# Kernel optimization log

Hardware: AMD Instinct MI355X
Metric: run time of the kernel (lower is better)

## Reference

```python
import jax, jax.numpy as jnp
import numpy as np

N_NODES = 100_000
N_EDGES = 1_600_000
N_GRAPHS = 256          # num_segments for batch scatter (static)
T_CAPS = 16             # num_target_cap
IN_CH = 64
OUT_CH = 64
NUM_ROUTES = 3
BN_EPS = 1e-5


def squash(s, axis=-1):
    # v = (|s|^2 / (1+|s|^2)) * s / |s|
    sq = jnp.sum(s * s, axis=axis, keepdims=True)
    return (sq / (1.0 + sq)) * s / jnp.sqrt(sq + 1e-16)


def setup_inputs() -> dict:
    key = jax.random.key(0)
    k_x, k_ei, k_ew, k_b, k_w, k_bias = jax.random.split(key, 6)
    x = jax.random.normal(k_x, (N_NODES, IN_CH), dtype=jnp.float32)
    edge_index = jax.random.randint(k_ei, (2, N_EDGES), 0, N_NODES, dtype=jnp.int32)
    edge_weight = jax.random.uniform(k_ew, (N_EDGES,), dtype=jnp.float32)
    batch = jnp.sort(jax.random.randint(k_b, (N_NODES,), 0, N_GRAPHS, dtype=jnp.int32))
    # per-capsule GCNConv weights, stacked: (T, in, out), bias (T, out)
    W = jax.random.normal(k_w, (T_CAPS, IN_CH, OUT_CH), dtype=jnp.float32) * 0.05
    bias = jax.random.normal(k_bias, (T_CAPS, OUT_CH), dtype=jnp.float32) * 0.05
    bn_gamma = jnp.ones((IN_CH,), dtype=jnp.float32)
    bn_beta = jnp.zeros((IN_CH,), dtype=jnp.float32)
    return {"x": x, "edge_index": edge_index, "edge_weight": edge_weight,
            "batch": batch, "bn_gamma": bn_gamma, "bn_beta": bn_beta,
            "W": W, "bias": bias}


def reference(x, edge_index, edge_weight, batch, bn_gamma, bn_beta, W, bias):
    N = x.shape[0]
    T = W.shape[0]
    # --- BatchNorm1d (training-mode batch statistics, biased variance) ---
    mu = jnp.mean(x, axis=0)
    var = jnp.var(x, axis=0)
    xn = (x - mu) * jax.lax.rsqrt(var + BN_EPS) * bn_gamma + bn_beta

    # --- GCNConv (shared graph): A_hat x, then per-capsule linear ---
    row, col = edge_index[0], edge_index[1]
    ar = jnp.arange(N, dtype=edge_index.dtype)
    row_f = jnp.concatenate([row, ar])              # add self-loops, weight 1
    col_f = jnp.concatenate([col, ar])
    w_f = jnp.concatenate([edge_weight, jnp.ones((N,), x.dtype)])
    deg = jax.ops.segment_sum(w_f, col_f, num_segments=N)
    dinv = jnp.where(deg > 0, jax.lax.rsqrt(deg), 0.0)
    norm = dinv[row_f] * w_f * dinv[col_f]          # (E+N,)
    h = jax.ops.segment_sum(norm[:, None] * xn[row_f], col_f, num_segments=N)  # (N, in)
    # linearity: propagate(A, x W_t) == (propagate(A, x)) W_t
    u_hat = jnp.einsum('ni,tio->nto', h, W) + bias[None]  # (N, T, D)

    # --- dynamic routing ---
    node_deg = jax.ops.segment_sum(edge_weight, row, num_segments=N)  # (N,)
    b_log = jnp.broadcast_to(node_deg[:, None, None], (N, T, 1))
    u_det = jax.lax.stop_gradient(u_hat)
    for _ in range(NUM_ROUTES - 1):
        c = jax.nn.softmax(b_log, axis=1)                         # (N, T, 1)
        s = jax.ops.segment_sum(c * u_det, batch, num_segments=N_GRAPHS)  # (G, T, D)
        v = squash(s, axis=-1)
        vg = v[batch]                                             # (N, T, D)
        b_log = b_log + jnp.sum(u_det * vg, axis=-1, keepdims=True)
    c = jax.nn.softmax(b_log, axis=1)
    s = jax.ops.segment_sum(c * u_hat, batch, num_segments=N_GRAPHS)  # (G, T, D)

    # --- add per-graph mean of (normalized) node features ---
    cnt = jax.ops.segment_sum(jnp.ones((N,), x.dtype), batch, num_segments=N_GRAPHS)
    x_mean = jax.ops.segment_sum(xn, batch, num_segments=N_GRAPHS) / jnp.maximum(cnt, 1.0)[:, None]
    s = s + x_mean[:, None, :]                                    # needs in==out
    v = squash(s, axis=-1)

    # --- final_layer=True: v.norm(p=-1, dim=-1) = (sum |v|^-1)^-1 ---
    out = 1.0 / jnp.sum(1.0 / jnp.abs(v), axis=-1)                # (G, T)
    return out
```

## Files before the change

### kernel.cpp

```cpp
#include <hip/hip_runtime.h>
#include <hip/hip_fp16.h>
#include <math.h>

#define N_NODES 100000
#define N_EDGES 1600000
#define N_GRAPHS 256
#define T_CAPS 16
#define D_CH 64
#define BN_EPS 1e-5f
#define NSPLIT 8
#define CHUNK 32
#define FIX_SCALE 33554432.0f

__device__ __forceinline__ float waveReduceSum(float v) {
    for (int m = 32; m >= 1; m >>= 1) v += __shfl_xor(v, m, 64);
    return v;
}

__global__ void setup_kernel(unsigned long long* pack, float* bn_sums, float* hsum, float* xsum,
                             const float* __restrict__ W, float* __restrict__ WT,
                             const int* __restrict__ batch, int* __restrict__ gstart) {
    int idx = blockIdx.x * blockDim.x + threadIdx.x;
    if (idx < N_NODES) pack[idx] = 0ULL;
    if (idx < 128) bn_sums[idx] = 0.0f;
    if (idx < N_GRAPHS * D_CH) { hsum[idx] = 0.0f; xsum[idx] = 0.0f; }
    if (idx < T_CAPS * 64 * 64) {
        int t = idx >> 12, rem = idx & 4095, o = rem >> 6, i = rem & 63;
        WT[idx] = W[t * 4096 + i * 64 + o];
    }
    if (idx <= N_GRAPHS) {
        int lo = 0, hi = N_NODES;
        while (lo < hi) { int mid = (lo + hi) >> 1; if (batch[mid] < idx) lo = mid + 1; else hi = mid; }
        gstart[idx] = lo;
    }
}

__global__ void bn_stats_kernel(const float* __restrict__ x, float* __restrict__ sums,
                                __half2* __restrict__ x16) {
    int pr = threadIdx.x & 31;
    int rg = threadIdx.x >> 5;
    int c0 = pr * 2;
    float s0 = 0, q0 = 0, s1 = 0, q1 = 0;
    for (int r = blockIdx.x * 8 + rg; r < N_NODES; r += gridDim.x * 8) {
        float2 v = *(const float2*)(x + (size_t)r * 64 + c0);
        s0 += v.x; q0 += v.x * v.x;
        s1 += v.y; q1 += v.y * v.y;
        x16[(size_t)r * 32 + pr] = __floats2half2_rn(v.x, v.y);
    }
    __shared__ float ls[2][8][64];
    ls[0][rg][c0] = s0; ls[0][rg][c0 + 1] = s1;
    ls[1][rg][c0] = q0; ls[1][rg][c0 + 1] = q1;
    __syncthreads();
    if (threadIdx.x < 64) {
        float a = 0.0f, b = 0.0f;
        for (int i = 0; i < 8; i++) { a += ls[0][i][threadIdx.x]; b += ls[1][i][threadIdx.x]; }
        atomicAdd(&sums[threadIdx.x], a);
        atomicAdd(&sums[64 + threadIdx.x], b);
    }
}

__global__ void hist_kernel(const int* __restrict__ col, const float* __restrict__ ew,
                            unsigned long long* __restrict__ pack, int* __restrict__ rank) {
    int e = blockIdx.x * blockDim.x + threadIdx.x;
    if (e >= N_EDGES) return;
    int c = col[e];
    unsigned fx = __float2uint_rn(ew[e] * FIX_SCALE);
    unsigned long long old = atomicAdd(&pack[c], (1ULL << 32) | (unsigned long long)fx);
    rank[e] = (int)(old >> 32);
}

__global__ void scan1_kernel(const unsigned long long* __restrict__ pack, int* __restrict__ off,
                             int* __restrict__ bsum, float* __restrict__ dinv,
                             const float* __restrict__ sums, const float* __restrict__ gamma,
                             const float* __restrict__ beta, float* __restrict__ ab) {
    __shared__ int lds[256];
    int tid = threadIdx.x;
    int base = blockIdx.x * 1024 + tid * 4;
    int c[4];
    #pragma unroll
    for (int i = 0; i < 4; i++) {
        if (base + i < N_NODES) {
            unsigned long long pv = pack[base + i];
            c[i] = (int)(pv >> 32);
            float d = 1.0f + (float)(unsigned)(pv & 0xFFFFFFFFULL) * (1.0f / FIX_SCALE);
            dinv[base + i] = 1.0f / sqrtf(d);
        } else c[i] = 0;
    }
    if (blockIdx.x == 0 && tid < 64) {
        float mu = sums[tid] * (1.0f / N_NODES);
        float var = sums[64 + tid] * (1.0f / N_NODES) - mu * mu;
        float inv = 1.0f / sqrtf(var + BN_EPS);
        float a = inv * gamma[tid];
        ab[tid] = a;
        ab[64 + tid] = beta[tid] - mu * a;
    }
    int tsum = c[0] + c[1] + c[2] + c[3];
    lds[tid] = tsum;
    __syncthreads();
    for (int d = 1; d < 256; d <<= 1) {
        int v = (tid >= d) ? lds[tid - d] : 0;
        __syncthreads();
        lds[tid] += v;
        __syncthreads();
    }
    int excl = lds[tid] - tsum;
    if (base + 0 < N_NODES) off[base + 0] = excl;
    if (base + 1 < N_NODES) off[base + 1] = excl + c[0];
    if (base + 2 < N_NODES) off[base + 2] = excl + c[0] + c[1];
    if (base + 3 < N_NODES) off[base + 3] = excl + c[0] + c[1] + c[2];
    if (tid == 255) bsum[blockIdx.x] = lds[255];
}

__global__ void scan2_kernel(int* __restrict__ bsum, int nb) {
    __shared__ int lds[128];
    int tid = threadIdx.x;
    int v = (tid < nb) ? bsum[tid] : 0;
    lds[tid] = v;
    __syncthreads();
    for (int d = 1; d < 128; d <<= 1) {
        int u = (tid >= d) ? lds[tid - d] : 0;
        __syncthreads();
        lds[tid] += u;
        __syncthreads();
    }
    if (tid < nb) bsum[tid] = lds[tid] - v;
}

__global__ void scan3_kernel(int* __restrict__ off, const int* __restrict__ bsum) {
    int idx = blockIdx.x * blockDim.x + threadIdx.x;
    if (idx < N_NODES) off[idx] = off[idx] + bsum[idx >> 10];
    if (idx == 0) off[N_NODES] = N_EDGES;
}

__global__ void scatter_kernel(const int* __restrict__ row, const int* __restrict__ col,
                               const float* __restrict__ ew, const int* __restrict__ rank,
                               const float* __restrict__ dinv, const int* __restrict__ off,
                               int2* __restrict__ rec) {
    int e = blockIdx.x * blockDim.x + threadIdx.x;
    if (e >= N_EDGES) return;
    int c = col[e], r = row[e];
    float coef = dinv[r] * ew[e] * dinv[c];
    int pos = off[c] + rank[e];
    rec[pos] = make_int2(r, __float_as_int(coef));
}

__global__ void h_gather_kernel(const int2* __restrict__ rec, const int* __restrict__ off,
                                const float* __restrict__ dinv, const __half* __restrict__ x16,
                                const float* __restrict__ ab, float* __restrict__ h) {
    int n = blockIdx.x * 4 + (threadIdx.x >> 6);
    int ch = threadIdx.x & 63;
    int e0 = off[n], e1 = off[n + 1];
    float dv = dinv[n];
    float cself = dv * dv;
    float acc0 = cself * __half2float(x16[(size_t)n * 64 + ch]);
    float acc1 = 0.0f, acc2 = 0.0f, acc3 = 0.0f;
    float csr = cself;
    int e = e0;
    for (; e + 4 <= e1; e += 4) {
        int2 r0 = rec[e], r1 = rec[e + 1], r2 = rec[e + 2], r3 = rec[e + 3];
        float c0 = __int_as_float(r0.y), c1 = __int_as_float(r1.y);
        float c2 = __int_as_float(r2.y), c3 = __int_as_float(r3.y);
        float x0 = __half2float(x16[(size_t)r0.x * 64 + ch]);
        float x1 = __half2float(x16[(size_t)r1.x * 64 + ch]);
        float x2 = __half2float(x16[(size_t)r2.x * 64 + ch]);
        float x3 = __half2float(x16[(size_t)r3.x * 64 + ch]);
        acc0 += c0 * x0; acc1 += c1 * x1; acc2 += c2 * x2; acc3 += c3 * x3;
        csr += c0 + c1 + c2 + c3;
    }
    for (; e < e1; ++e) {
        int2 rc = rec[e];
        float c = __int_as_float(rc.y);
        acc0 += c * __half2float(x16[(size_t)rc.x * 64 + ch]);
        csr += c;
    }
    float acc = (acc0 + acc1) + (acc2 + acc3);
    h[(size_t)n * 64 + ch] = ab[ch] * acc + ab[64 + ch] * csr;
}

__global__ void gsum_kernel(const __half* __restrict__ x16, const float* __restrict__ h,
                            const int* __restrict__ gstart, float* __restrict__ xsum,
                            float* __restrict__ hsum) {
    int g = blockIdx.x / NSPLIT, sp = blockIdx.x % NSPLIT;
    int s0g = gstart[g], s1g = gstart[g + 1];
    int len = s1g - s0g;
    int q = (len + NSPLIT - 1) / NSPLIT;
    int a0 = s0g + sp * q, a1 = min(s1g, a0 + q);
    int ch = threadIdx.x & 63, rg = threadIdx.x >> 6;
    float ax = 0.0f, ah = 0.0f;
    for (int n = a0 + rg; n < a1; n += 4) {
        ax += __half2float(x16[(size_t)n * 64 + ch]);
        ah += h[(size_t)n * 64 + ch];
    }
    __shared__ float lx[4][64], lh[4][64];
    lx[rg][ch] = ax; lh[rg][ch] = ah;
    __syncthreads();
    if (threadIdx.x < 64) {
        int c = threadIdx.x;
        float sx = lx[0][c] + lx[1][c] + lx[2][c] + lx[3][c];
        float sh = lh[0][c] + lh[1][c] + lh[2][c] + lh[3][c];
        atomicAdd(&xsum[g * 64 + c], sx);
        atomicAdd(&hsum[g * 64 + c], sh);
    }
}

__global__ void ka_fused_kernel(const float* __restrict__ h, const int* __restrict__ gstart,
                                const float* __restrict__ wva, const float* __restrict__ bva,
                                const float* __restrict__ wvb, const float* __restrict__ bvb,
                                float* __restrict__ hc_part, float* __restrict__ csum_part,
                                int mode) {
    int g = blockIdx.x / NSPLIT, sp = blockIdx.x % NSPLIT;
    int s0g = gstart[g], s1g = gstart[g + 1];
    int len = s1g - s0g;
    int q = (len + NSPLIT - 1) / NSPLIT;
    int s0 = s0g + sp * q, s1 = min(s1g, s0 + q);
    int tid = threadIdx.x;
    int d = tid & 63, tg = tid >> 6;
    int t = tid & 15, kh = tid >> 4;

    __shared__ float hlds[CHUNK][65];
    __shared__ float wa[16][65];
    __shared__ float wb[16][65];
    __shared__ float clds[CHUNK][17];
    __shared__ float bvl[2][16];

    for (int i = tid; i < 16 * 64; i += 256) {
        int tt = i >> 6, dd = i & 63;
        wa[tt][dd] = wva[(g * 16 + tt) * 64 + dd];
        if (mode) wb[tt][dd] = wvb[(g * 16 + tt) * 64 + dd];
    }
    if (tid < 16) { bvl[0][tid] = bva[g * 16 + tid]; bvl[1][tid] = mode ? bvb[g * 16 + tid] : 0.0f; }
    for (int i = tid; i < CHUNK * 65; i += 256) ((float*)hlds)[i] = 0.0f;
    __syncthreads();

    float acc0 = 0, acc1 = 0, acc2 = 0, acc3 = 0;
    float cs0 = 0, cs1 = 0, cs2 = 0, cs3 = 0;

    for (int n0 = s0; n0 < s1; n0 += CHUNK) {
        int nn = min(CHUNK, s1 - n0);
        #pragma unroll
        for (int j = 0; j < 8; j++) {
            int k = tg * 8 + j;
            if (k < nn) hlds[k][d] = h[(size_t)(n0 + k) * 64 + d];
        }
        __syncthreads();
        int k0 = kh, k1 = kh + 16;
        float u0, u1;
        if (mode) {
            float a0 = bvl[0][t], a1 = bvl[0][t], b0 = bvl[1][t], b1 = bvl[1][t];
            for (int dd = 0; dd < 64; dd++) {
                float wav = wa[t][dd], wbv = wb[t][dd];
                float h0 = hlds[k0][dd], h1 = hlds[k1][dd];
                a0 += h0 * wav; a1 += h1 * wav;
                b0 += h0 * wbv; b1 += h1 * wbv;
            }
            u0 = a0 + b0; u1 = a1 + b1;
        } else {
            float a0 = bvl[0][t], a1 = bvl[0][t];
            for (int dd = 0; dd < 64; dd++) {
                float wav = wa[t][dd];
                a0 += hlds[k0][dd] * wav; a1 += hlds[k1][dd] * wav;
            }
            u0 = a0; u1 = a1;
        }
        float m0 = u0, m1 = u1;
        #pragma unroll
        for (int msk = 1; msk < 16; msk <<= 1) {
            m0 = fmaxf(m0, __shfl_xor(m0, msk, 64));
            m1 = fmaxf(m1, __shfl_xor(m1, msk, 64));
        }
        float e0 = expf(u0 - m0), e1 = expf(u1 - m1);
        float z0 = e0, z1 = e1;
        #pragma unroll
        for (int msk = 1; msk < 16; msk <<= 1) {
            z0 += __shfl_xor(z0, msk, 64);
            z1 += __shfl_xor(z1, msk, 64);
        }
        if (k0 < nn) clds[k0][t] = e0 / z0;
        if (k1 < nn) clds[k1][t] = e1 / z1;
        __syncthreads();
        for (int k = 0; k < nn; k++) {
            float hv = hlds[k][d];
            float c0 = clds[k][tg * 4 + 0], c1 = clds[k][tg * 4 + 1];
            float c2 = clds[k][tg * 4 + 2], c3 = clds[k][tg * 4 + 3];
            acc0 += c0 * hv; acc1 += c1 * hv; acc2 += c2 * hv; acc3 += c3 * hv;
            if (d == 0) { cs0 += c0; cs1 += c1; cs2 += c2; cs3 += c3; }
        }
        __syncthreads();
    }
    size_t base = ((size_t)(sp * N_GRAPHS + g) * 16 + tg * 4) * 64 + d;
    hc_part[base] = acc0; hc_part[base + 64] = acc1;
    hc_part[base + 128] = acc2; hc_part[base + 192] = acc3;
    if (d == 0) {
        int cb = (sp * N_GRAPHS + g) * 16 + tg * 4;
        csum_part[cb + 0] = cs0; csum_part[cb + 1] = cs1;
        csum_part[cb + 2] = cs2; csum_part[cb + 3] = cs3;
    }
}

__global__ void kb_kernel(const float* __restrict__ hsum, const float* __restrict__ hc_part,
                          const float* __restrict__ csum_part, const float* __restrict__ W,
                          const float* __restrict__ WT, const float* __restrict__ bias,
                          const float* __restrict__ xsum, const float* __restrict__ ab,
                          const int* __restrict__ gstart, float* __restrict__ wv,
                          float* __restrict__ bv, float* __restrict__ out, int mode) {
    int wid = blockIdx.x * 4 + (threadIdx.x >> 6);
    int lane = threadIdx.x & 63;
    int g = wid >> 4, t = wid & 15;
    const float* Wt = W + t * 4096;
    float cnt = (float)(gstart[g + 1] - gstart[g]);
    float s;
    if (mode == 0) {
        const float* hr = hsum + g * 64;
        float acc = cnt * bias[t * 64 + lane];
        for (int i = 0; i < 64; i++) acc += hr[i] * Wt[i * 64 + lane];
        s = acc * (1.0f / 16.0f);
    } else {
        float csum = 0.0f;
        #pragma unroll
        for (int sp = 0; sp < NSPLIT; sp++) csum += csum_part[(sp * N_GRAPHS + g) * 16 + t];
        float acc = csum * bias[t * 64 + lane];
        for (int i = 0; i < 64; i++) {
            float hci = 0.0f;
            #pragma unroll
            for (int sp = 0; sp < NSPLIT; sp++)
                hci += hc_part[((size_t)(sp * N_GRAPHS + g) * 16 + t) * 64 + i];
            acc += hci * Wt[i * 64 + lane];
        }
        s = acc;
        if (mode == 2) {
            float xm = ab[lane] * xsum[g * 64 + lane] / fmaxf(cnt, 1.0f) + ab[64 + lane];
            s += xm;
        }
    }
    float sq = waveReduceSum(s * s);
    float scale = (sq / (1.0f + sq)) / sqrtf(sq + 1e-16f);
    float v = scale * s;
    if (mode == 2) {
        float tot = waveReduceSum(1.0f / fabsf(v));
        if (lane == 0) out[wid] = 1.0f / tot;
    } else {
        __shared__ float vlds[4][64];
        int w = threadIdx.x >> 6;
        vlds[w][lane] = v;
        __syncthreads();
        const float* WTt = WT + t * 4096;
        float acc = 0.0f;
        for (int o = 0; o < 64; o++) acc += WTt[o * 64 + lane] * vlds[w][o];
        wv[(size_t)wid * 64 + lane] = acc;
        float b = waveReduceSum(bias[t * 64 + lane] * v);
        if (lane == 0) bv[wid] = b;
    }
}

extern "C" void kernel_launch(void* const* d_in, const int* in_sizes, int n_in,
                              void* d_out, int out_size, void* d_ws, size_t ws_size,
                              hipStream_t stream) {
    const float* x     = (const float*)d_in[0];
    const int*   ei    = (const int*)d_in[1];
    const float* ew    = (const float*)d_in[2];
    const int*   batch = (const int*)d_in[3];
    const float* gamma = (const float*)d_in[4];
    const float* beta  = (const float*)d_in[5];
    const float* W     = (const float*)d_in[6];
    const float* bias  = (const float*)d_in[7];
    float* out = (float*)d_out;

    const int* row = ei;
    const int* col = ei + N_EDGES;

    char* basep = (char*)d_ws;
    int2* rec = (int2*)basep;                              basep += sizeof(int2) * N_EDGES;
    unsigned long long* pack = (unsigned long long*)basep; basep += 8ULL * N_NODES;
    __half2* x16 = (__half2*)basep;                        basep += 2ULL * N_NODES * D_CH;
    float* p = (float*)basep;
    float* h        = p; p += (size_t)N_NODES * D_CH;
    float* hc_part  = p; p += (size_t)NSPLIT * N_GRAPHS * T_CAPS * D_CH;
    float* csum_part= p; p += NSPLIT * N_GRAPHS * T_CAPS;
    float* wva      = p; p += N_GRAPHS * T_CAPS * D_CH;
    float* bva      = p; p += N_GRAPHS * T_CAPS;
    float* wvb      = p; p += N_GRAPHS * T_CAPS * D_CH;
    float* bvb      = p; p += N_GRAPHS * T_CAPS;
    float* WT       = p; p += T_CAPS * 64 * 64;
    float* dinv     = p; p += N_NODES;
    float* bn_sums  = p; p += 128;
    float* ab       = p; p += 128;
    float* hsum     = p; p += N_GRAPHS * D_CH;
    float* xsum     = p; p += N_GRAPHS * D_CH;
    int*   ip       = (int*)p;
    int*   off      = ip; ip += N_NODES + 1;
    int*   rank     = ip; ip += N_EDGES;
    int*   bsum     = ip; ip += 128;
    int*   gstart   = ip; ip += N_GRAPHS + 1;

    const int nscan = (N_NODES + 1023) / 1024;

    setup_kernel<<<(N_NODES + 255) / 256, 256, 0, stream>>>(pack, bn_sums, hsum, xsum,
                                                             W, WT, batch, gstart);
    bn_stats_kernel<<<512, 256, 0, stream>>>(x, bn_sums, x16);
    hist_kernel<<<(N_EDGES + 255) / 256, 256, 0, stream>>>(col, ew, pack, rank);
    scan1_kernel<<<nscan, 256, 0, stream>>>(pack, off, bsum, dinv, bn_sums, gamma, beta, ab);
    scan2_kernel<<<1, 128, 0, stream>>>(bsum, nscan);
    scan3_kernel<<<(N_NODES + 255) / 256, 256, 0, stream>>>(off, bsum);
    scatter_kernel<<<(N_EDGES + 255) / 256, 256, 0, stream>>>(row, col, ew, rank, dinv, off, rec);
    h_gather_kernel<<<N_NODES / 4, 256, 0, stream>>>(rec, off, dinv, (const __half*)x16, ab, h);
    gsum_kernel<<<N_GRAPHS * NSPLIT, 256, 0, stream>>>((const __half*)x16, h, gstart, xsum, hsum);

    kb_kernel<<<N_GRAPHS * T_CAPS / 4, 256, 0, stream>>>(hsum, hc_part, csum_part, W, WT, bias,
                                                          xsum, ab, gstart, wva, bva, out, 0);
    ka_fused_kernel<<<N_GRAPHS * NSPLIT, 256, 0, stream>>>(h, gstart, wva, bva, wvb, bvb,
                                                            hc_part, csum_part, 0);
    kb_kernel<<<N_GRAPHS * T_CAPS / 4, 256, 0, stream>>>(hsum, hc_part, csum_part, W, WT, bias,
                                                          xsum, ab, gstart, wvb, bvb, out, 1);
    ka_fused_kernel<<<N_GRAPHS * NSPLIT, 256, 0, stream>>>(h, gstart, wva, bva, wvb, bvb,
                                                            hc_part, csum_part, 1);
    kb_kernel<<<N_GRAPHS * T_CAPS / 4, 256, 0, stream>>>(hsum, hc_part, csum_part, W, WT, bias,
                                                          xsum, ab, gstart, wva, bva, out, 2);
}
```

Baseline: 341.8 us.

## Privatize degree histogram into partitions and fuse BN stats into hist launch

The per-node degree/count atomic histogram is split into 8 partition copies chosen by block index, which spreads out atomic contention. The scan now combines the partitions into per-partition offsets used by the scatter. The BatchNorm statistics pass is merged into the same launch as extra blocks, so one launch is removed and the two independent passes can overlap. In exchange, the scan and setup passes read and write 8x more pack/offset memory.

New measurement: 336.1 us. Within noise of the previous version (-1.7%).

```diff
diff --git a/kernel.cpp b/kernel.cpp
--- a/kernel.cpp
+++ b/kernel.cpp
@@ -10,7 +10,10 @@
 #define BN_EPS 1e-5f
 #define NSPLIT 8
 #define CHUNK 32
+#define NPART 8
+#define NBN 512
 #define FIX_SCALE 33554432.0f
+#define HIST_BLOCKS (N_EDGES / 256)
 
 __device__ __forceinline__ float waveReduceSum(float v) {
     for (int m = 32; m >= 1; m >>= 1) v += __shfl_xor(v, m, 64);
@@ -21,7 +24,7 @@
                              const float* __restrict__ W, float* __restrict__ WT,
                              const int* __restrict__ batch, int* __restrict__ gstart) {
     int idx = blockIdx.x * blockDim.x + threadIdx.x;
-    if (idx < N_NODES) pack[idx] = 0ULL;
+    if (idx < NPART * N_NODES) pack[idx] = 0ULL;
     if (idx < 128) bn_sums[idx] = 0.0f;
     if (idx < N_GRAPHS * D_CH) { hsum[idx] = 0.0f; xsum[idx] = 0.0f; }
     if (idx < T_CAPS * 64 * 64) {
@@ -35,56 +38,69 @@
     }
 }
 
-__global__ void bn_stats_kernel(const float* __restrict__ x, float* __restrict__ sums,
-                                __half2* __restrict__ x16) {
-    int pr = threadIdx.x & 31;
-    int rg = threadIdx.x >> 5;
-    int c0 = pr * 2;
-    float s0 = 0, q0 = 0, s1 = 0, q1 = 0;
-    for (int r = blockIdx.x * 8 + rg; r < N_NODES; r += gridDim.x * 8) {
-        float2 v = *(const float2*)(x + (size_t)r * 64 + c0);
-        s0 += v.x; q0 += v.x * v.x;
-        s1 += v.y; q1 += v.y * v.y;
-        x16[(size_t)r * 32 + pr] = __floats2half2_rn(v.x, v.y);
-    }
-    __shared__ float ls[2][8][64];
-    ls[0][rg][c0] = s0; ls[0][rg][c0 + 1] = s1;
-    ls[1][rg][c0] = q0; ls[1][rg][c0 + 1] = q1;
-    __syncthreads();
-    if (threadIdx.x < 64) {
-        float a = 0.0f, b = 0.0f;
-        for (int i = 0; i < 8; i++) { a += ls[0][i][threadIdx.x]; b += ls[1][i][threadIdx.x]; }
-        atomicAdd(&sums[threadIdx.x], a);
-        atomicAdd(&sums[64 + threadIdx.x], b);
-    }
-}
-
-__global__ void hist_kernel(const int* __restrict__ col, const float* __restrict__ ew,
-                            unsigned long long* __restrict__ pack, int* __restrict__ rank) {
-    int e = blockIdx.x * blockDim.x + threadIdx.x;
-    if (e >= N_EDGES) return;
-    int c = col[e];
-    unsigned fx = __float2uint_rn(ew[e] * FIX_SCALE);
-    unsigned long long old = atomicAdd(&pack[c], (1ULL << 32) | (unsigned long long)fx);
-    rank[e] = (int)(old >> 32);
+__global__ void histbn_kernel(const int* __restrict__ col, const float* __restrict__ ew,
+                              unsigned long long* __restrict__ pack, int* __restrict__ rank,
+                              const float* __restrict__ x, float* __restrict__ sums,
+                              __half2* __restrict__ x16) {
+    int b = blockIdx.x;
+    if (b < HIST_BLOCKS) {
+        int e = b * 256 + threadIdx.x;
+        int c = col[e];
+        unsigned fx = __float2uint_rn(ew[e] * FIX_SCALE);
+        size_t slot = (size_t)(b & (NPART - 1)) * N_NODES + c;
+        unsigned long long old = atomicAdd(&pack[slot], (1ULL << 32) | (unsigned long long)fx);
+        rank[e] = (int)(old >> 32);
+    } else {
+        int bb = b - HIST_BLOCKS;
+        int pr = threadIdx.x & 31;
+        int rg = threadIdx.x >> 5;
+        int c0 = pr * 2;
+        float s0 = 0, q0 = 0, s1 = 0, q1 = 0;
+        for (int r = bb * 8 + rg; r < N_NODES; r += NBN * 8) {
+            float2 v = *(const float2*)(x + (size_t)r * 64 + c0);
+            s0 += v.x; q0 += v.x * v.x;
+            s1 += v.y; q1 += v.y * v.y;
+            x16[(size_t)r * 32 + pr] = __floats2half2_rn(v.x, v.y);
+        }
+        __shared__ float ls[2][8][64];
+        ls[0][rg][c0] = s0; ls[0][rg][c0 + 1] = s1;
+        ls[1][rg][c0] = q0; ls[1][rg][c0 + 1] = q1;
+        __syncthreads();
+        if (threadIdx.x < 64) {
+            float a = 0.0f, bsum = 0.0f;
+            for (int i = 0; i < 8; i++) { a += ls[0][i][threadIdx.x]; bsum += ls[1][i][threadIdx.x]; }
+            atomicAdd(&sums[threadIdx.x], a);
+            atomicAdd(&sums[64 + threadIdx.x], bsum);
+        }
+    }
 }
 
 __global__ void scan1_kernel(const unsigned long long* __restrict__ pack, int* __restrict__ off,
-                             int* __restrict__ bsum, float* __restrict__ dinv,
-                             const float* __restrict__ sums, const float* __restrict__ gamma,
-                             const float* __restrict__ beta, float* __restrict__ ab) {
+                             int* __restrict__ bsum, int* __restrict__ poff,
+                             float* __restrict__ dinv, const float* __restrict__ sums,
+                             const float* __restrict__ gamma, const float* __restrict__ beta,
+                             float* __restrict__ ab) {
     __shared__ int lds[256];
     int tid = threadIdx.x;
     int base = blockIdx.x * 1024 + tid * 4;
-    int c[4];
+    int tot[4];
     #pragma unroll
     for (int i = 0; i < 4; i++) {
-        if (base + i < N_NODES) {
-            unsigned long long pv = pack[base + i];
-            c[i] = (int)(pv >> 32);
-            float d = 1.0f + (float)(unsigned)(pv & 0xFFFFFFFFULL) * (1.0f / FIX_SCALE);
-            dinv[base + i] = 1.0f / sqrtf(d);
-        } else c[i] = 0;
+        int c = base + i;
+        if (c < N_NODES) {
+            unsigned run = 0;
+            unsigned long long low_total = 0;
+            #pragma unroll
+            for (int p = 0; p < NPART; p++) {
+                unsigned long long pv = pack[(size_t)p * N_NODES + c];
+                poff[(size_t)p * N_NODES + c] = (int)run;
+                run += (unsigned)(pv >> 32);
+                low_total += (pv & 0xFFFFFFFFULL);
+            }
+            tot[i] = (int)run;
+            float d = 1.0f + (float)low_total * (1.0f / FIX_SCALE);
+            dinv[c] = 1.0f / sqrtf(d);
+        } else tot[i] = 0;
     }
     if (blockIdx.x == 0 && tid < 64) {
         float mu = sums[tid] * (1.0f / N_NODES);
@@ -94,7 +110,7 @@
         ab[tid] = a;
         ab[64 + tid] = beta[tid] - mu * a;
     }
-    int tsum = c[0] + c[1] + c[2] + c[3];
+    int tsum = tot[0] + tot[1] + tot[2] + tot[3];
     lds[tid] = tsum;
     __syncthreads();
     for (int d = 1; d < 256; d <<= 1) {
@@ -105,9 +121,9 @@
     }
     int excl = lds[tid] - tsum;
     if (base + 0 < N_NODES) off[base + 0] = excl;
-    if (base + 1 < N_NODES) off[base + 1] = excl + c[0];
-    if (base + 2 < N_NODES) off[base + 2] = excl + c[0] + c[1];
-    if (base + 3 < N_NODES) off[base + 3] = excl + c[0] + c[1] + c[2];
+    if (base + 1 < N_NODES) off[base + 1] = excl + tot[0];
+    if (base + 2 < N_NODES) off[base + 2] = excl + tot[0] + tot[1];
+    if (base + 3 < N_NODES) off[base + 3] = excl + tot[0] + tot[1] + tot[2];
     if (tid == 255) bsum[blockIdx.x] = lds[255];
 }
 
@@ -126,21 +142,28 @@
     if (tid < nb) bsum[tid] = lds[tid] - v;
 }
 
-__global__ void scan3_kernel(int* __restrict__ off, const int* __restrict__ bsum) {
+__global__ void scan3_kernel(int* __restrict__ off, const int* __restrict__ bsum,
+                             int* __restrict__ poff) {
     int idx = blockIdx.x * blockDim.x + threadIdx.x;
-    if (idx < N_NODES) off[idx] = off[idx] + bsum[idx >> 10];
+    if (idx < N_NODES) {
+        int o = off[idx] + bsum[idx >> 10];
+        off[idx] = o;
+        #pragma unroll
+        for (int p = 0; p < NPART; p++) poff[(size_t)p * N_NODES + idx] += o;
+    }
     if (idx == 0) off[N_NODES] = N_EDGES;
 }
 
 __global__ void scatter_kernel(const int* __restrict__ row, const int* __restrict__ col,
                                const float* __restrict__ ew, const int* __restrict__ rank,
-                               const float* __restrict__ dinv, const int* __restrict__ off,
+                               const float* __restrict__ dinv, const int* __restrict__ poff,
                                int2* __restrict__ rec) {
     int e = blockIdx.x * blockDim.x + threadIdx.x;
     if (e >= N_EDGES) return;
     int c = col[e], r = row[e];
+    int p = (e >> 8) & (NPART - 1);
     float coef = dinv[r] * ew[e] * dinv[c];
-    int pos = off[c] + rank[e];
+    int pos = poff[(size_t)p * N_NODES + c] + rank[e];
     rec[pos] = make_int2(r, __float_as_int(coef));
 }
 
@@ -370,7 +393,7 @@
 
     char* basep = (char*)d_ws;
     int2* rec = (int2*)basep;                              basep += sizeof(int2) * N_EDGES;
-    unsigned long long* pack = (unsigned long long*)basep; basep += 8ULL * N_NODES;
+    unsigned long long* pack = (unsigned long long*)basep; basep += 8ULL * NPART * N_NODES;
     __half2* x16 = (__half2*)basep;                        basep += 2ULL * N_NODES * D_CH;
     float* p = (float*)basep;
     float* h        = p; p += (size_t)N_NODES * D_CH;
@@ -389,19 +412,19 @@
     int*   ip       = (int*)p;
     int*   off      = ip; ip += N_NODES + 1;
     int*   rank     = ip; ip += N_EDGES;
+    int*   poff     = ip; ip += NPART * N_NODES;
     int*   bsum     = ip; ip += 128;
     int*   gstart   = ip; ip += N_GRAPHS + 1;
 
     const int nscan = (N_NODES + 1023) / 1024;
 
-    setup_kernel<<<(N_NODES + 255) / 256, 256, 0, stream>>>(pack, bn_sums, hsum, xsum,
-                                                             W, WT, batch, gstart);
-    bn_stats_kernel<<<512, 256, 0, stream>>>(x, bn_sums, x16);
-    hist_kernel<<<(N_EDGES + 255) / 256, 256, 0, stream>>>(col, ew, pack, rank);
-    scan1_kernel<<<nscan, 256, 0, stream>>>(pack, off, bsum, dinv, bn_sums, gamma, beta, ab);
+    setup_kernel<<<(NPART * N_NODES + 255) / 256, 256, 0, stream>>>(pack, bn_sums, hsum, xsum,
+                                                                     W, WT, batch, gstart);
+    histbn_kernel<<<HIST_BLOCKS + NBN, 256, 0, stream>>>(col, ew, pack, rank, x, bn_sums, x16);
+    scan1_kernel<<<nscan, 256, 0, stream>>>(pack, off, bsum, poff, dinv, bn_sums, gamma, beta, ab);
     scan2_kernel<<<1, 128, 0, stream>>>(bsum, nscan);
-    scan3_kernel<<<(N_NODES + 255) / 256, 256, 0, stream>>>(off, bsum);
-    scatter_kernel<<<(N_EDGES + 255) / 256, 256, 0, stream>>>(row, col, ew, rank, dinv, off, rec);
+    scan3_kernel<<<(N_NODES + 255) / 256, 256, 0, stream>>>(off, bsum, poff);
+    scatter_kernel<<<(N_EDGES + 255) / 256, 256, 0, stream>>>(row, col, ew, rank, dinv, poff, rec);
     h_gather_kernel<<<N_NODES / 4, 256, 0, stream>>>(rec, off, dinv, (const __half*)x16, ab, h);
     gsum_kernel<<<N_GRAPHS * NSPLIT, 256, 0, stream>>>((const __half*)x16, h, gstart, xsum, hsum);
 
```

## Replace global-atomic CSR build with two-level bucketed counting sort

Applied to the files above, without the earlier changes.

Rebuilds the CSR construction as a two-level counting sort. Edges are first histogrammed per 4096-edge block into 128-node buckets in shared memory, then scanned and scattered into bucket order. Each bucket is then sorted locally with shared-memory atomics, which also accumulate degrees and produce dinv and offsets. This replaces per-edge 64-bit global atomics and the rank array with mostly shared-memory atomics and more coalesced writes. The histogram pass is fused with the BN stats pass, and edge coefficients are now computed inside the gather. That adds an extra dinv load per edge there, plus an extra pass over a bucketed edge buffer.

New measurement: 279.0 us. 18.4% less time.

```diff
diff --git a/kernel.cpp b/kernel.cpp
--- a/kernel.cpp
+++ b/kernel.cpp
@@ -11,17 +11,20 @@
 #define NSPLIT 8
 #define CHUNK 32
 #define FIX_SCALE 33554432.0f
+#define NB 782
+#define EPB 4096
+#define NBLK 391
+#define NBN 512
 
 __device__ __forceinline__ float waveReduceSum(float v) {
     for (int m = 32; m >= 1; m >>= 1) v += __shfl_xor(v, m, 64);
     return v;
 }
 
-__global__ void setup_kernel(unsigned long long* pack, float* bn_sums, float* hsum, float* xsum,
+__global__ void setup_kernel(float* bn_sums, float* hsum, float* xsum,
                              const float* __restrict__ W, float* __restrict__ WT,
                              const int* __restrict__ batch, int* __restrict__ gstart) {
     int idx = blockIdx.x * blockDim.x + threadIdx.x;
-    if (idx < N_NODES) pack[idx] = 0ULL;
     if (idx < 128) bn_sums[idx] = 0.0f;
     if (idx < N_GRAPHS * D_CH) { hsum[idx] = 0.0f; xsum[idx] = 0.0f; }
     if (idx < T_CAPS * 64 * 64) {
@@ -35,67 +38,56 @@
     }
 }
 
-__global__ void bn_stats_kernel(const float* __restrict__ x, float* __restrict__ sums,
+__global__ void passA_bn_kernel(const int* __restrict__ col, int* __restrict__ gh,
+                                const float* __restrict__ x, float* __restrict__ sums,
                                 __half2* __restrict__ x16) {
-    int pr = threadIdx.x & 31;
-    int rg = threadIdx.x >> 5;
-    int c0 = pr * 2;
-    float s0 = 0, q0 = 0, s1 = 0, q1 = 0;
-    for (int r = blockIdx.x * 8 + rg; r < N_NODES; r += gridDim.x * 8) {
-        float2 v = *(const float2*)(x + (size_t)r * 64 + c0);
-        s0 += v.x; q0 += v.x * v.x;
-        s1 += v.y; q1 += v.y * v.y;
-        x16[(size_t)r * 32 + pr] = __floats2half2_rn(v.x, v.y);
-    }
-    __shared__ float ls[2][8][64];
-    ls[0][rg][c0] = s0; ls[0][rg][c0 + 1] = s1;
-    ls[1][rg][c0] = q0; ls[1][rg][c0 + 1] = q1;
-    __syncthreads();
-    if (threadIdx.x < 64) {
-        float a = 0.0f, b = 0.0f;
-        for (int i = 0; i < 8; i++) { a += ls[0][i][threadIdx.x]; b += ls[1][i][threadIdx.x]; }
-        atomicAdd(&sums[threadIdx.x], a);
-        atomicAdd(&sums[64 + threadIdx.x], b);
-    }
-}
-
-__global__ void hist_kernel(const int* __restrict__ col, const float* __restrict__ ew,
-                            unsigned long long* __restrict__ pack, int* __restrict__ rank) {
-    int e = blockIdx.x * blockDim.x + threadIdx.x;
-    if (e >= N_EDGES) return;
-    int c = col[e];
-    unsigned fx = __float2uint_rn(ew[e] * FIX_SCALE);
-    unsigned long long old = atomicAdd(&pack[c], (1ULL << 32) | (unsigned long long)fx);
-    rank[e] = (int)(old >> 32);
-}
-
-__global__ void scan1_kernel(const unsigned long long* __restrict__ pack, int* __restrict__ off,
-                             int* __restrict__ bsum, float* __restrict__ dinv,
-                             const float* __restrict__ sums, const float* __restrict__ gamma,
-                             const float* __restrict__ beta, float* __restrict__ ab) {
+    int blk = blockIdx.x;
+    int tid = threadIdx.x;
+    if (blk < NBLK) {
+        __shared__ unsigned hist[NB];
+        for (int j = tid; j < NB; j += 256) hist[j] = 0u;
+        __syncthreads();
+        #pragma unroll
+        for (int i = 0; i < EPB / 256; i++) {
+            int e = blk * EPB + i * 256 + tid;
+            if (e < N_EDGES) atomicAdd(&hist[col[e] >> 7], 1u);
+        }
+        __syncthreads();
+        for (int j = tid; j < NB; j += 256) gh[blk * NB + j] = (int)hist[j];
+    } else {
+        int bb = blk - NBLK;
+        int pr = tid & 31;
+        int rg = tid >> 5;
+        int c0 = pr * 2;
+        float s0 = 0, q0 = 0, s1 = 0, q1 = 0;
+        for (int r = bb * 8 + rg; r < N_NODES; r += NBN * 8) {
+            float2 v = *(const float2*)(x + (size_t)r * 64 + c0);
+            s0 += v.x; q0 += v.x * v.x;
+            s1 += v.y; q1 += v.y * v.y;
+            x16[(size_t)r * 32 + pr] = __floats2half2_rn(v.x, v.y);
+        }
+        __shared__ float ls[2][8][64];
+        ls[0][rg][c0] = s0; ls[0][rg][c0 + 1] = s1;
+        ls[1][rg][c0] = q0; ls[1][rg][c0 + 1] = q1;
+        __syncthreads();
+        if (tid < 64) {
+            float a = 0.0f, bsm = 0.0f;
+            for (int i = 0; i < 8; i++) { a += ls[0][i][tid]; bsm += ls[1][i][tid]; }
+            atomicAdd(&sums[tid], a);
+            atomicAdd(&sums[64 + tid], bsm);
+        }
+    }
+}
+
+__global__ void passB1_kernel(int* __restrict__ gh, int* __restrict__ Tarr) {
+    int b = blockIdx.x;
+    int tid = threadIdx.x;
     __shared__ int lds[256];
-    int tid = threadIdx.x;
-    int base = blockIdx.x * 1024 + tid * 4;
-    int c[4];
-    #pragma unroll
-    for (int i = 0; i < 4; i++) {
-        if (base + i < N_NODES) {
-            unsigned long long pv = pack[base + i];
-            c[i] = (int)(pv >> 32);
-            float d = 1.0f + (float)(unsigned)(pv & 0xFFFFFFFFULL) * (1.0f / FIX_SCALE);
-            dinv[base + i] = 1.0f / sqrtf(d);
-        } else c[i] = 0;
-    }
-    if (blockIdx.x == 0 && tid < 64) {
-        float mu = sums[tid] * (1.0f / N_NODES);
-        float var = sums[64 + tid] * (1.0f / N_NODES) - mu * mu;
-        float inv = 1.0f / sqrtf(var + BN_EPS);
-        float a = inv * gamma[tid];
-        ab[tid] = a;
-        ab[64 + tid] = beta[tid] - mu * a;
-    }
-    int tsum = c[0] + c[1] + c[2] + c[3];
-    lds[tid] = tsum;
+    int i0 = tid * 2, i1 = tid * 2 + 1;
+    int v0 = (i0 < NBLK) ? gh[(size_t)i0 * NB + b] : 0;
+    int v1 = (i1 < NBLK) ? gh[(size_t)i1 * NB + b] : 0;
+    int pair = v0 + v1;
+    lds[tid] = pair;
     __syncthreads();
     for (int d = 1; d < 256; d <<= 1) {
         int v = (tid >= d) ? lds[tid - d] : 0;
@@ -103,45 +95,107 @@
         lds[tid] += v;
         __syncthreads();
     }
+    int excl = lds[tid] - pair;
+    if (i0 < NBLK) gh[(size_t)i0 * NB + b] = excl;
+    if (i1 < NBLK) gh[(size_t)i1 * NB + b] = excl + v0;
+    if (tid == 255) Tarr[b] = lds[255];
+}
+
+__global__ void passB2_kernel(const int* __restrict__ Tarr, int* __restrict__ Sarr,
+                              int* __restrict__ off) {
+    __shared__ int lds[256];
+    int tid = threadIdx.x;
+    int base = tid * 4;
+    int t0 = (base + 0 < NB) ? Tarr[base + 0] : 0;
+    int t1 = (base + 1 < NB) ? Tarr[base + 1] : 0;
+    int t2 = (base + 2 < NB) ? Tarr[base + 2] : 0;
+    int t3 = (base + 3 < NB) ? Tarr[base + 3] : 0;
+    int tsum = t0 + t1 + t2 + t3;
+    lds[tid] = tsum;
+    __syncthreads();
+    for (int d = 1; d < 256; d <<= 1) {
+        int v = (tid >= d) ? lds[tid - d] : 0;
+        __syncthreads();
+        lds[tid] += v;
+        __syncthreads();
+    }
     int excl = lds[tid] - tsum;
-    if (base + 0 < N_NODES) off[base + 0] = excl;
-    if (base + 1 < N_NODES) off[base + 1] = excl + c[0];
-    if (base + 2 < N_NODES) off[base + 2] = excl + c[0] + c[1];
-    if (base + 3 < N_NODES) off[base + 3] = excl + c[0] + c[1] + c[2];
-    if (tid == 255) bsum[blockIdx.x] = lds[255];
-}
-
-__global__ void scan2_kernel(int* __restrict__ bsum, int nb) {
-    __shared__ int lds[128];
-    int tid = threadIdx.x;
-    int v = (tid < nb) ? bsum[tid] : 0;
-    lds[tid] = v;
+    if (base + 0 < NB) Sarr[base + 0] = excl;
+    if (base + 1 < NB) Sarr[base + 1] = excl + t0;
+    if (base + 2 < NB) Sarr[base + 2] = excl + t0 + t1;
+    if (base + 3 < NB) Sarr[base + 3] = excl + t0 + t1 + t2;
+    if (tid == 0) { Sarr[NB] = N_EDGES; off[N_NODES] = N_EDGES; }
+}
+
+__global__ void passC_kernel(const int* __restrict__ row, const int* __restrict__ col,
+                             const float* __restrict__ ew, const int* __restrict__ gh,
+                             const int* __restrict__ Sarr, int2* __restrict__ brec) {
+    int blk = blockIdx.x;
+    int tid = threadIdx.x;
+    __shared__ int cur[NB];
+    for (int j = tid; j < NB; j += 256) cur[j] = Sarr[j] + gh[(size_t)blk * NB + j];
+    __syncthreads();
+    #pragma unroll
+    for (int i = 0; i < EPB / 256; i++) {
+        int e = blk * EPB + i * 256 + tid;
+        if (e < N_EDGES) {
+            int c = col[e], r = row[e];
+            float w = ew[e];
+            int b = c >> 7;
+            int pos = atomicAdd(&cur[b], 1);
+            brec[pos] = make_int2(((c & 127) << 17) | r, __float_as_int(w));
+        }
+    }
+}
+
+__global__ void passD_kernel(const int2* __restrict__ brec, const int* __restrict__ Sarr,
+                             float* __restrict__ dinv, int* __restrict__ off,
+                             int2* __restrict__ rec) {
+    int b = blockIdx.x;
+    int tid = threadIdx.x;
+    int s0 = Sarr[b], s1 = Sarr[b + 1];
+    __shared__ unsigned cnt[128];
+    __shared__ unsigned degfx[128];
+    __shared__ int scan_tmp[128];
+    __shared__ int cOff[128];
+    __shared__ int cursor[128];
+    if (tid < 128) { cnt[tid] = 0u; degfx[tid] = 0u; }
+    __syncthreads();
+    for (int e = s0 + tid; e < s1; e += 256) {
+        int2 rc = brec[e];
+        int cl = (rc.x >> 17) & 127;
+        atomicAdd(&cnt[cl], 1u);
+        unsigned fx = __float2uint_rn(__int_as_float(rc.y) * FIX_SCALE);
+        atomicAdd(&degfx[cl], fx);
+    }
+    __syncthreads();
+    if (tid < 128) scan_tmp[tid] = (int)cnt[tid];
     __syncthreads();
     for (int d = 1; d < 128; d <<= 1) {
-        int u = (tid >= d) ? lds[tid - d] : 0;
-        __syncthreads();
-        lds[tid] += u;
-        __syncthreads();
-    }
-    if (tid < nb) bsum[tid] = lds[tid] - v;
-}
-
-__global__ void scan3_kernel(int* __restrict__ off, const int* __restrict__ bsum) {
-    int idx = blockIdx.x * blockDim.x + threadIdx.x;
-    if (idx < N_NODES) off[idx] = off[idx] + bsum[idx >> 10];
-    if (idx == 0) off[N_NODES] = N_EDGES;
-}
-
-__global__ void scatter_kernel(const int* __restrict__ row, const int* __restrict__ col,
-                               const float* __restrict__ ew, const int* __restrict__ rank,
-                               const float* __restrict__ dinv, const int* __restrict__ off,
-                               int2* __restrict__ rec) {
-    int e = blockIdx.x * blockDim.x + threadIdx.x;
-    if (e >= N_EDGES) return;
-    int c = col[e], r = row[e];
-    float coef = dinv[r] * ew[e] * dinv[c];
-    int pos = off[c] + rank[e];
-    rec[pos] = make_int2(r, __float_as_int(coef));
+        int v = 0;
+        if (tid < 128 && tid >= d) v = scan_tmp[tid - d];
+        __syncthreads();
+        if (tid < 128) scan_tmp[tid] += v;
+        __syncthreads();
+    }
+    if (tid < 128) {
+        int excl = scan_tmp[tid] - (int)cnt[tid];
+        cOff[tid] = excl;
+        cursor[tid] = excl;
+        int cg = b * 128 + tid;
+        if (cg < N_NODES) {
+            float d = 1.0f + (float)degfx[tid] * (1.0f / FIX_SCALE);
+            dinv[cg] = 1.0f / sqrtf(d);
+            off[cg] = s0 + excl;
+        }
+    }
+    __syncthreads();
+    for (int e = s0 + tid; e < s1; e += 256) {
+        int2 rc = brec[e];
+        int cl = (rc.x >> 17) & 127;
+        int pos = atomicAdd((unsigned*)&cursor[cl], 1u);
+        rec[s0 + (int)pos] = make_int2(rc.x & 0x1FFFF, rc.y);
+    }
 }
 
 __global__ void h_gather_kernel(const int2* __restrict__ rec, const int* __restrict__ off,
@@ -158,8 +212,10 @@
     int e = e0;
     for (; e + 4 <= e1; e += 4) {
         int2 r0 = rec[e], r1 = rec[e + 1], r2 = rec[e + 2], r3 = rec[e + 3];
-        float c0 = __int_as_float(r0.y), c1 = __int_as_float(r1.y);
-        float c2 = __int_as_float(r2.y), c3 = __int_as_float(r3.y);
+        float c0 = dinv[r0.x] * __int_as_float(r0.y) * dv;
+        float c1 = dinv[r1.x] * __int_as_float(r1.y) * dv;
+        float c2 = dinv[r2.x] * __int_as_float(r2.y) * dv;
+        float c3 = dinv[r3.x] * __int_as_float(r3.y) * dv;
         float x0 = __half2float(x16[(size_t)r0.x * 64 + ch]);
         float x1 = __half2float(x16[(size_t)r1.x * 64 + ch]);
         float x2 = __half2float(x16[(size_t)r2.x * 64 + ch]);
@@ -169,12 +225,25 @@
     }
     for (; e < e1; ++e) {
         int2 rc = rec[e];
-        float c = __int_as_float(rc.y);
+        float c = dinv[rc.x] * __int_as_float(rc.y) * dv;
         acc0 += c * __half2float(x16[(size_t)rc.x * 64 + ch]);
         csr += c;
     }
     float acc = (acc0 + acc1) + (acc2 + acc3);
     h[(size_t)n * 64 + ch] = ab[ch] * acc + ab[64 + ch] * csr;
+}
+
+__global__ void ab_kernel(const float* __restrict__ sums, const float* __restrict__ gamma,
+                          const float* __restrict__ beta, float* __restrict__ ab) {
+    int tid = threadIdx.x;
+    if (tid < 64) {
+        float mu = sums[tid] * (1.0f / N_NODES);
+        float var = sums[64 + tid] * (1.0f / N_NODES) - mu * mu;
+        float inv = 1.0f / sqrtf(var + BN_EPS);
+        float a = inv * gamma[tid];
+        ab[tid] = a;
+        ab[64 + tid] = beta[tid] - mu * a;
+    }
 }
 
 __global__ void gsum_kernel(const __half* __restrict__ x16, const float* __restrict__ h,
@@ -369,9 +438,9 @@
     const int* col = ei + N_EDGES;
 
     char* basep = (char*)d_ws;
-    int2* rec = (int2*)basep;                              basep += sizeof(int2) * N_EDGES;
-    unsigned long long* pack = (unsigned long long*)basep; basep += 8ULL * N_NODES;
-    __half2* x16 = (__half2*)basep;                        basep += 2ULL * N_NODES * D_CH;
+    int2* rec  = (int2*)basep;                     basep += sizeof(int2) * N_EDGES;
+    int2* brec = (int2*)basep;                     basep += sizeof(int2) * N_EDGES;
+    __half2* x16 = (__half2*)basep;                basep += 2ULL * N_NODES * D_CH;
     float* p = (float*)basep;
     float* h        = p; p += (size_t)N_NODES * D_CH;
     float* hc_part  = p; p += (size_t)NSPLIT * N_GRAPHS * T_CAPS * D_CH;
@@ -388,20 +457,19 @@
     float* xsum     = p; p += N_GRAPHS * D_CH;
     int*   ip       = (int*)p;
     int*   off      = ip; ip += N_NODES + 1;
-    int*   rank     = ip; ip += N_EDGES;
-    int*   bsum     = ip; ip += 128;
+    int*   gh       = ip; ip += (size_t)NBLK * NB;
+    int*   Tarr     = ip; ip += NB;
+    int*   Sarr     = ip; ip += NB + 1;
     int*   gstart   = ip; ip += N_GRAPHS + 1;
 
-    const int nscan = (N_NODES + 1023) / 1024;
-
-    setup_kernel<<<(N_NODES + 255) / 256, 256, 0, stream>>>(pack, bn_sums, hsum, xsum,
-                                                             W, WT, batch, gstart);
-    bn_stats_kernel<<<512, 256, 0, stream>>>(x, bn_sums, x16);
-    hist_kernel<<<(N_EDGES + 255) / 256, 256, 0, stream>>>(col, ew, pack, rank);
-    scan1_kernel<<<nscan, 256, 0, stream>>>(pack, off, bsum, dinv, bn_sums, gamma, beta, ab);
-    scan2_kernel<<<1, 128, 0, stream>>>(bsum, nscan);
-    scan3_kernel<<<(N_NODES + 255) / 256, 256, 0, stream>>>(off, bsum);
-    scatter_kernel<<<(N_EDGES + 255) / 256, 256, 0, stream>>>(row, col, ew, rank, dinv, off, rec);
+    setup_kernel<<<(T_CAPS * 64 * 64 + 255) / 256, 256, 0, stream>>>(bn_sums, hsum, xsum,
+                                                                      W, WT, batch, gstart);
+    passA_bn_kernel<<<NBLK + NBN, 256, 0, stream>>>(col, gh, x, bn_sums, x16);
+    ab_kernel<<<1, 64, 0, stream>>>(bn_sums, gamma, beta, ab);
+    passB1_kernel<<<NB, 256, 0, stream>>>(gh, Tarr);
+    passB2_kernel<<<1, 256, 0, stream>>>(Tarr, Sarr, off);
+    passC_kernel<<<NBLK, 256, 0, stream>>>(row, col, ew, gh, Sarr, brec);
+    passD_kernel<<<NB, 256, 0, stream>>>(brec, Sarr, dinv, off, rec);
     h_gather_kernel<<<N_NODES / 4, 256, 0, stream>>>(rec, off, dinv, (const __half*)x16, ab, h);
     gsum_kernel<<<N_GRAPHS * NSPLIT, 256, 0, stream>>>((const __half*)x16, h, gstart, xsum, hsum);
 
```
